# Optimization experiments

Hardware: AMD Instinct MI355X
Metric: run time of the kernel (lower is better)

The kernel has to match this reference:

```python
import jax, jax.numpy as jnp
import numpy as np

DIM, HEADS, B, HT, WD = 96, 8, 4, 160, 160


def conv2d(x, w, b=None, padding=0, groups=1):
    out = jax.lax.conv_general_dilated(
        x, w, (1, 1), [(padding, padding), (padding, padding)],
        dimension_numbers=('NCHW', 'OIHW', 'NCHW'), feature_group_count=groups)
    if b is not None:
        out = out + b[None, :, None, None]
    return out


def setup_inputs() -> dict:
    key = jax.random.key(0)
    ks = jax.random.split(key, 16)
    dim, H = DIM, HEADS
    p = lambda i, shape: jax.random.normal(ks[i], shape, jnp.float32) * 0.05
    return {
        'x': jax.random.normal(ks[0], (B, dim, HT, WD), jnp.float32),
        'spectral': jax.random.normal(ks[1], (B, dim), jnp.float32),
        'temperature': jnp.ones((H, 1, 1), jnp.float32),
        'w_qkv': p(2, (3 * dim, dim, 1, 1)),           # 1x1x1 conv3d == 1x1 conv2d (depth=1)
        'w_dw': p(3, (3 * dim, 1, 3, 3)),              # middle depth slice of 3x3x3 dwconv
        'w_proj': p(4, (dim, dim, 1, 1)),
        'w_fc': p(5, (9, 3 * H)), 'b_fc': jnp.zeros((9,), jnp.float32),
        'w_dep': p(6, (dim, 9, 3, 3)), 'b_dep': jnp.zeros((dim,), jnp.float32),
        'w_se1': p(7, (2 * dim, dim)), 'b_se1': jnp.zeros((2 * dim,), jnp.float32),
        'w_se2': p(8, (dim, 2 * dim)), 'b_se2': jnp.zeros((dim,), jnp.float32),
        'w_saw1': p(9, (dim // 4, 1, 3, 3)), 'b_saw1': jnp.zeros((dim // 4,), jnp.float32),
        'w_saw2': p(10, (HEADS, dim // 4, 1, 1)), 'b_saw2': jnp.zeros((HEADS,), jnp.float32),
        'w_sgp': p(11, (dim, dim)), 'b_sgp': jnp.zeros((dim,), jnp.float32),
    }


def reference(x, spectral, temperature, w_qkv, w_dw, w_proj, w_fc, b_fc,
              w_dep, b_dep, w_se1, b_se1, w_se2, b_se2,
              w_saw1, b_saw1, w_saw2, b_saw2, w_sgp, b_sgp):
    b, c, h, w = x.shape
    H = temperature.shape[0]
    cH = c // H
    # spectral enhance gate: Linear -> GELU -> Linear -> Sigmoid
    sw = jax.nn.sigmoid(
        jax.nn.gelu(spectral @ w_se1.T + b_se1, approximate=False) @ w_se2.T + b_se2)
    x = x * sw[:, :, None, None]
    # qkv: 1x1 conv then 3x3 depthwise (depth-1 3D conv collapses to 2D middle slice)
    qkv = conv2d(conv2d(x, w_qkv), w_dw, padding=1, groups=3 * c)  # (b,3c,h,w)
    # fc branch: reshape (b,3c,h,w) -> (b,hw,3H,cH) -> (b,3H,hw,cH); 1x1 conv over 3H
    f_all = qkv.reshape(b, h * w, 3 * H, cH).transpose(0, 2, 1, 3)
    f_all = jnp.einsum('oc,bcnd->bond', w_fc, f_all) + b_fc[None, :, None, None]  # (b,9,hw,cH)
    f_conv = f_all.transpose(0, 3, 1, 2).reshape(b, 9 * cH, h, w)
    out_conv = conv2d(f_conv, w_dep, b_dep, padding=1, groups=cH)  # (b,c,h,w)
    # channel attention path
    q, k, v = jnp.split(qkv, 3, axis=1)
    resh = lambda t: t.reshape(b, H, cH, h * w)
    q, k, v = resh(q), resh(k), resh(v)
    sg = (spectral @ w_sgp.T + b_sgp).reshape(b, H, cH)
    cm = x.mean(axis=(1, 2, 3), keepdims=True)                      # (b,1,1,1)
    cm_exp = jnp.broadcast_to(cm, (b, 1, h, w))
    saw = jax.nn.sigmoid(conv2d(
        jax.nn.gelu(conv2d(cm_exp, w_saw1, b_saw1, padding=1), approximate=False),
        w_saw2, b_saw2))                                            # (b,H,h,w)
    saw = saw.mean(axis=(2, 3))[..., None]                          # (b,H,1)
    esg = sg * saw                                                  # (b,H,cH)
    sgm = esg[..., :, None] * esg[..., None, :]                     # (b,H,cH,cH)
    qn = q / jnp.maximum(jnp.linalg.norm(q, axis=-1, keepdims=True), 1e-12)
    kn = k / jnp.maximum(jnp.linalg.norm(k, axis=-1, keepdims=True), 1e-12)
    attn = jnp.einsum('bhcn,bhdn->bhcd', qn, kn) * temperature[None]
    attn = jax.nn.softmax(attn * sgm, axis=-1)
    out = jnp.einsum('bhcd,bhdn->bhcn', attn, v).reshape(b, c, h, w)
    out = conv2d(out, w_proj)
    return out + out_conv
```

## Files before the change

### kernel.cpp

```cpp
#include <hip/hip_runtime.h>
#include <math.h>

#define NB 4
#define C 96
#define C3 288
#define NH 8
#define CHD 12
#define HT 160
#define WD 160
#define HW 25600

typedef unsigned short u16;
typedef unsigned int   u32;
typedef __bf16 bf16x8 __attribute__((ext_vector_type(8)));
typedef float  f32x4  __attribute__((ext_vector_type(4)));

__device__ __forceinline__ float gelu_f(float x){
    return 0.5f * x * (1.0f + erff(x * 0.7071067811865475f));
}
__device__ __forceinline__ float sigmoid_f(float x){
    return 1.0f / (1.0f + expf(-x));
}
__device__ __forceinline__ u16 f2bf(float x){
    union { float f; u32 u; } v; v.f = x;
    u32 r = v.u + 0x7FFFu + ((v.u >> 16) & 1u);
    return (u16)(r >> 16);
}
__device__ __forceinline__ float bf2f(u16 s){
    union { u32 u; float f; } v; v.u = ((u32)s) << 16;
    return v.f;
}

__global__ __launch_bounds__(256) void k0_xsum(const float* __restrict__ x,
                                               float* __restrict__ xsum,
                                               u16* __restrict__ xb){
    int bc = blockIdx.x;
    const float4* p4 = (const float4*)(x + (size_t)bc * HW);
    u32* xo = (u32*)(xb + (size_t)bc * HW);
    float s = 0.f;
    for (int i = threadIdx.x; i < HW/4; i += 256){
        float4 v = p4[i];
        s += (v.x + v.y) + (v.z + v.w);
        xo[i*2]   = (u32)f2bf(v.x) | ((u32)f2bf(v.y) << 16);
        xo[i*2+1] = (u32)f2bf(v.z) | ((u32)f2bf(v.w) << 16);
    }
    __shared__ float red[256];
    red[threadIdx.x] = s;
    __syncthreads();
    for (int off = 128; off > 0; off >>= 1){
        if (threadIdx.x < off) red[threadIdx.x] += red[threadIdx.x + off];
        __syncthreads();
    }
    if (threadIdx.x == 0) xsum[bc] = red[0];
}

__global__ void k1_small(const float* __restrict__ spectral, const float* __restrict__ xsum,
                         const float* __restrict__ w_se1, const float* __restrict__ b_se1,
                         const float* __restrict__ w_se2, const float* __restrict__ b_se2,
                         const float* __restrict__ w_saw1, const float* __restrict__ b_saw1,
                         const float* __restrict__ w_saw2, const float* __restrict__ b_saw2,
                         const float* __restrict__ w_sgp, const float* __restrict__ b_sgp,
                         float* __restrict__ swg, float* __restrict__ esgg){
    __shared__ float spec[96];
    __shared__ float h1[192];
    __shared__ float cm_s;
    __shared__ float g1[9][24];
    __shared__ float saw[8];
    __shared__ float redbuf[96];
    int t = threadIdx.x;
    int b = blockIdx.x;
    if (t < 96) spec[t] = spectral[b*96 + t];
    __syncthreads();
    if (t < 192){
        float a = b_se1[t];
        for (int c = 0; c < 96; c++) a += spec[c] * w_se1[t*96 + c];
        h1[t] = gelu_f(a);
    }
    __syncthreads();
    if (t < 96){
        float a = b_se2[t];
        for (int j = 0; j < 192; j++) a += h1[j] * w_se2[t*192 + j];
        float s = sigmoid_f(a);
        swg[b*96 + t] = s;
        redbuf[t] = s * xsum[b*96 + t];
    }
    __syncthreads();
    if (t == 0){
        float cs = 0.f;
        for (int c = 0; c < 96; c++) cs += redbuf[c];
        cm_s = cs / (96.0f * (float)HW);
    }
    __syncthreads();
    float cm = cm_s;
    if (t < 9*24){
        int cat = t / 24, ch = t % 24;
        int ti = cat / 3, tj = cat % 3;
        float S = 0.f;
        for (int ki = 0; ki < 3; ki++){
            if (ti == 0 && ki == 0) continue;
            if (ti == 2 && ki == 2) continue;
            for (int kj = 0; kj < 3; kj++){
                if (tj == 0 && kj == 0) continue;
                if (tj == 2 && kj == 2) continue;
                S += w_saw1[ch*9 + ki*3 + kj];
            }
        }
        g1[cat][ch] = gelu_f(cm * S + b_saw1[ch]);
    }
    __syncthreads();
    if (t < 8){
        float acc = 0.f;
        const float cnt[3] = {1.f, 158.f, 1.f};
        for (int cat = 0; cat < 9; cat++){
            float a = b_saw2[t];
            for (int ch = 0; ch < 24; ch++) a += w_saw2[t*24 + ch] * g1[cat][ch];
            acc += cnt[cat/3] * cnt[cat%3] * sigmoid_f(a);
        }
        saw[t] = acc / (float)HW;
    }
    __syncthreads();
    if (t < 96){
        float a = b_sgp[t];
        for (int j = 0; j < 96; j++) a += spec[j] * w_sgp[t*96 + j];
        esgg[b*96 + t] = a * saw[t/12];
    }
}

__global__ __launch_bounds__(256) void k1w_weff(const float* __restrict__ w_qkv,
                                                const float* __restrict__ swg,
                                                u16* __restrict__ weffb){
    int b = blockIdx.x;
    int i = blockIdx.y * 256 + threadIdx.x;
    float w = w_qkv[i] * swg[b*96 + (i % 96)];
    weffb[(size_t)b*C3*96 + i] = f2bf(w);
}

__global__ __launch_bounds__(384) void k2a_mfma(const u16* __restrict__ xb,
                                                const u16* __restrict__ weffb,
                                                u16* __restrict__ Y,
                                                int bbase, long ystride){
    int b   = bbase + blockIdx.y;
    int px0 = blockIdx.x * 64;
    __shared__ u16 Xl[64*128];
    int t = threadIdx.x;
    const u32* xsrc = (const u32*)(xb + (size_t)b*C*HW + px0);
    for (int i = t; i < 96*32; i += 384){
        int c = i >> 5, pq = i & 31;
        u32 v = xsrc[(size_t)c*(HW/2) + pq];
        int slot = (((c >> 3) ^ (pq & 7)) << 3) + (c & 7);
        Xl[(2*pq)*128 + slot]     = (u16)(v & 0xffffu);
        Xl[(2*pq+1)*128 + slot]   = (u16)(v >> 16);
    }
    int wid = t >> 6, lane = t & 63;
    int lr = lane & 15, lk = lane >> 4;
    union U { uint4 q; bf16x8 v; };
    bf16x8 afr[3][3];
    const u16* wb = weffb + (size_t)b*C3*96;
    #pragma unroll
    for (int og = 0; og < 3; og++){
        int oc = og*96 + wid*16 + lr;
        #pragma unroll
        for (int kk = 0; kk < 3; kk++){
            U u; u.q = *(const uint4*)(wb + (size_t)oc*96 + kk*32 + lk*8);
            afr[og][kk] = u.v;
        }
    }
    __syncthreads();
    u16* Yb = Y + (size_t)blockIdx.y * ystride;
    #pragma unroll
    for (int sub = 0; sub < 4; sub++){
        int px = sub*16 + lr;
        int key = (px >> 1) & 7;
        bf16x8 bfr[3];
        #pragma unroll
        for (int kk = 0; kk < 3; kk++){
            int gs = (kk*4 + lk) ^ key;
            U u; u.q = *(const uint4*)(&Xl[px*128 + gs*8]);
            bfr[kk] = u.v;
        }
        #pragma unroll
        for (int og = 0; og < 3; og++){
            f32x4 acc = (f32x4){0.f,0.f,0.f,0.f};
            #pragma unroll
            for (int kk = 0; kk < 3; kk++)
                acc = __builtin_amdgcn_mfma_f32_16x16x32_bf16(afr[og][kk], bfr[kk], acc, 0, 0, 0);
            #pragma unroll
            for (int r = 0; r < 4; r++){
                int oc = og*96 + wid*16 + lk*4 + r;
                Yb[(size_t)oc*HW + px0 + sub*16 + lr] = f2bf(acc[r]);
            }
        }
    }
}

__global__ __launch_bounds__(256) void k2b_dw(const u16* __restrict__ Y,
                                              const float* __restrict__ w_dw,
                                              u16* __restrict__ qkv,
                                              int bbase, long ystride){
    int b  = bbase + blockIdx.z;
    int ch = blockIdx.y;
    int r0 = blockIdx.x * 8;
    __shared__ float tile[10*162];
    const u16* Yc = Y + (size_t)blockIdx.z*ystride + (size_t)ch*HW;
    int t = threadIdx.x;
    if (t < 10){ tile[t*162] = 0.f; tile[t*162 + 161] = 0.f; }
    for (int i = t; i < 800; i += 256){
        int r = i / 80, c2 = (i % 80) * 2;
        int gr = r0 + r - 1;
        u32 v = 0;
        if (gr >= 0 && gr < HT) v = *(const u32*)(Yc + gr*WD + c2);
        tile[r*162 + 1 + c2] = bf2f((u16)(v & 0xffffu));
        tile[r*162 + 2 + c2] = bf2f((u16)(v >> 16));
    }
    float w[9];
    #pragma unroll
    for (int k = 0; k < 9; k++) w[k] = w_dw[ch*9 + k];
    __syncthreads();
    u16* qc = qkv + ((size_t)b*C3 + ch)*HW + r0*WD;
    for (int i = t; i < 640; i += 256){
        int r = i / 80, c2 = (i % 80) * 2;
        float a0 = 0.f, a1 = 0.f;
        #pragma unroll
        for (int ki = 0; ki < 3; ki++){
            const float* row = &tile[(r+ki)*162 + c2];
            #pragma unroll
            for (int kj = 0; kj < 3; kj++){
                float wv = w[ki*3+kj];
                a0 += wv * row[kj];
                a1 += wv * row[kj+1];
            }
        }
        u32 pk = (u32)f2bf(a0) | ((u32)f2bf(a1) << 16);
        *(u32*)(qc + r*WD + c2) = pk;
    }
}

__global__ __launch_bounds__(256) void k3_mfma(const u16* __restrict__ qkv,
                                               const float* __restrict__ w_fc,
                                               const float* __restrict__ b_fc,
                                               u16* __restrict__ fws){
    int b  = blockIdx.y;
    int n0 = blockIdx.x * 64;
    __shared__ float wfc[216];
    __shared__ float bfc[9];
    __shared__ u16 ot[112*66];
    int t = threadIdx.x;
    if (t < 216) wfc[t] = w_fc[t];
    if (t < 9)   bfc[t] = b_fc[t];
    __syncthreads();
    int wv = t >> 6, lane = t & 63;
    int lr = lane & 15, lk = lane >> 4;
    int nrow = n0 + wv*16 + lr;
    const u16* rowp = qkv + (size_t)b*C3*HW + (size_t)nrow*288;
    union U { uint4 q; bf16x8 v; };
    U bfr[9];
    #pragma unroll
    for (int kk = 0; kk < 9; kk++)
        bfr[kk].q = *(const uint4*)(rowp + kk*32 + lk*8);

    for (int ct = 0; ct < 7; ct++){
        int coA = ct*16 + lr;
        int dA = coA / 9;
        int oA = coA - dA*9;
        f32x4 acc;
        #pragma unroll
        for (int r = 0; r < 4; r++){
            int coD = ct*16 + lk*4 + r;
            acc[r] = (coD < 108) ? bfc[coD % 9] : 0.f;
        }
        #pragma unroll
        for (int kk = 0; kk < 9; kk++){
            int base = kk*32 + lk*8;
            int bm = base % 12;
            int slot = dA - bm; slot += (slot < 0) ? 12 : 0;
            int j = base + slot;
            float wvl = (coA < 108 && slot < 8) ? wfc[oA*24 + j/12] : 0.f;
            u32 pk = ((u32)f2bf(wvl)) << ((slot & 1) * 16);
            int sh = slot >> 1;
            U a;
            a.q.x = (sh == 0) ? pk : 0u;
            a.q.y = (sh == 1) ? pk : 0u;
            a.q.z = (sh == 2) ? pk : 0u;
            a.q.w = (sh == 3) ? pk : 0u;
            acc = __builtin_amdgcn_mfma_f32_16x16x32_bf16(a.v, bfr[kk].v, acc, 0, 0, 0);
        }
        #pragma unroll
        for (int r = 0; r < 4; r++){
            int co = ct*16 + lk*4 + r;
            if (co < 108) ot[co*66 + wv*16 + lr] = f2bf(acc[r]);
        }
    }
    __syncthreads();
    const u32* otp = (const u32*)ot;
    u32* dst = (u32*)(fws + (size_t)b*108*HW + n0);
    for (int i = t; i < 108*32; i += 256){
        int pl = i >> 5, q = i & 31;
        dst[(size_t)pl*(HW/2) + q] = otp[pl*33 + q];
    }
}

__global__ __launch_bounds__(256) void k4_gram(const u16* __restrict__ qkv,
                                               float* __restrict__ gpart){
    int b = blockIdx.z;
    int h = blockIdx.y;
    int t = threadIdx.x;
    __shared__ float qs[12*268];
    __shared__ float ks[12*268];
    const u32* qu = (const u32*)(qkv + ((size_t)b*C3 + h*CHD)*HW + blockIdx.x*1024);
    const u32* ku = (const u32*)(qkv + ((size_t)b*C3 + C + h*CHD)*HW + blockIdx.x*1024);
    float acc = 0.f;
    for (int sc = 0; sc < 4; sc++){
        __syncthreads();
        for (int i = t; i < 12*128; i += 256){
            int rr = i / 128, pu = i % 128;
            u32 qv = qu[rr*(HW/2) + sc*128 + pu];
            u32 kv = ku[rr*(HW/2) + sc*128 + pu];
            qs[rr*268 + 2*pu]     = bf2f((u16)(qv & 0xffffu));
            qs[rr*268 + 2*pu + 1] = bf2f((u16)(qv >> 16));
            ks[rr*268 + 2*pu]     = bf2f((u16)(kv & 0xffffu));
            ks[rr*268 + 2*pu + 1] = bf2f((u16)(kv >> 16));
        }
        __syncthreads();
        if (t < 144){
            int c = t / 12, d = t % 12;
            const float* qq = &qs[c*268];
            const float* kk = &ks[d*268];
            float a = 0.f;
            for (int p = 0; p < 256; p += 4){
                float4 q4 = *(const float4*)(qq + p);
                float4 k4 = *(const float4*)(kk + p);
                a += q4.x*k4.x + q4.y*k4.y + q4.z*k4.z + q4.w*k4.w;
            }
            acc += a;
        } else if (t < 168){
            int c = (t - 144) % 12;
            const float* qq = (t < 156) ? &qs[c*268] : &ks[c*268];
            float a = 0.f;
            for (int p = 0; p < 256; p += 4){
                float4 q4 = *(const float4*)(qq + p);
                a += q4.x*q4.x + q4.y*q4.y + q4.z*q4.z + q4.w*q4.w;
            }
            acc += a;
        }
    }
    if (t < 168)
        gpart[(((size_t)b*NH + h)*25 + blockIdx.x)*168 + t] = acc;
}

__global__ void k5_attn(const float* __restrict__ gpart, const float* __restrict__ esgg,
                        const float* __restrict__ temp, const float* __restrict__ w_proj,
                        u16* __restrict__ Mhib, u16* __restrict__ Mlob){
    int b = blockIdx.x;
    int t = threadIdx.x;
    __shared__ float G[NH][144];
    __shared__ float q2[NH][12], k2[NH][12];
    __shared__ float attn[NH][144];
    for (int i = t; i < NH*168; i += 256){
        int h = i / 168, e = i % 168;
        float a = 0.f;
        for (int ch = 0; ch < 25; ch++)
            a += gpart[(((size_t)b*NH + h)*25 + ch)*168 + e];
        if (e < 144)      G[h][e] = a;
        else if (e < 156) q2[h][e-144] = a;
        else              k2[h][e-156] = a;
    }
    __syncthreads();
    if (t < 96){
        int h = t / 12, c = t % 12;
        float rq  = 1.0f / fmaxf(sqrtf(q2[h][c]), 1e-12f);
        float tm  = temp[h];
        float egc = esgg[b*96 + h*12 + c];
        float lo[12];
        float mx = -1e30f;
        for (int d = 0; d < 12; d++){
            float rk = 1.0f / fmaxf(sqrtf(k2[h][d]), 1e-12f);
            float v = G[h][c*12 + d] * rq * rk * tm * (egc * esgg[b*96 + h*12 + d]);
            lo[d] = v;
            mx = fmaxf(mx, v);
        }
        float s = 0.f;
        for (int d = 0; d < 12; d++){ lo[d] = expf(lo[d] - mx); s += lo[d]; }
        float inv = 1.0f / s;
        for (int d = 0; d < 12; d++) attn[h][c*12 + d] = lo[d] * inv;
    }
    __syncthreads();
    for (int i = t; i < 96*96; i += 256){
        int co = i / 96, ci = i % 96;
        int h = ci / 12, d = ci % 12;
        float a = 0.f;
        #pragma unroll
        for (int c = 0; c < 12; c++)
            a += w_proj[co*96 + h*12 + c] * attn[h][c*12 + d];
        u16 hi = f2bf(a);
        float resid = a - bf2f(hi);
        Mhib[((size_t)b*96 + co)*96 + ci] = hi;
        Mlob[((size_t)b*96 + co)*96 + ci] = f2bf(resid);
    }
}

#define K6_ST 35
#define K6_RT 18
__global__ __launch_bounds__(256) void k6a_mfma(const u16* __restrict__ fws,
                                                const float* __restrict__ w_dep,
                                                const float* __restrict__ b_dep,
                                                float* __restrict__ out){
    int b = blockIdx.z, d = blockIdx.y;
    int ty = blockIdx.x / 5, tx = blockIdx.x % 5;
    int r0 = ty*16, c0 = tx*32;
    __shared__ u16 inl[9*K6_RT*K6_ST];
    __shared__ u16 Wt[16*104];
    __shared__ float bb[8];
    int t = threadIdx.x;
    for (int i = t; i < 9*K6_RT*34; i += 256){
        int ch = i / (K6_RT*34), rem = i % (K6_RT*34), r = rem / 34, cc = rem % 34;
        int gr = r0 + r - 1, gc = c0 + cc - 1;
        u16 v = 0;
        if (gr >= 0 && gr < HT && gc >= 0 && gc < WD)
            v = fws[((size_t)(b*108 + d*9 + ch))*HW + gr*WD + gc];
        inl[(ch*K6_RT + r)*K6_ST + cc] = v;
    }
    for (int i = t; i < 16*96; i += 256){
        int row = i / 96, k = i % 96;
        float wv = (row < 8 && k < 81) ? w_dep[(d*8 + row)*81 + k] : 0.f;
        Wt[row*104 + k] = f2bf(wv);
    }
    if (t < 8) bb[t] = b_dep[d*8 + t];
    __syncthreads();

    int wv = t >> 6, lane = t & 63;
    int lr = lane & 15, lk = lane >> 4;
    union U { uint4 q; bf16x8 v; };
    bf16x8 afr[3];
    #pragma unroll
    for (int kk = 0; kk < 3; kk++){
        U u; u.q = *(const uint4*)(&Wt[lr*104 + kk*32 + lk*8]);
        afr[kk] = u.v;
    }
    int off[3][8];
    #pragma unroll
    for (int kk = 0; kk < 3; kk++)
        #pragma unroll
        for (int j = 0; j < 8; j++){
            int k = kk*32 + lk*8 + j;
            off[kk][j] = (k < 81) ? ((k/9)*K6_RT + (k%9)/3)*K6_ST + (k%3) : 0;
        }
    float binit[4];
    #pragma unroll
    for (int r = 0; r < 4; r++) binit[r] = (lk < 2) ? bb[lk*4 + r] : 0.f;

    for (int gi = 0; gi < 8; gi++){
        int g = wv*8 + gi;
        int ry = g >> 1, half = g & 1;
        int base = ry*K6_ST + half*16 + lr;
        f32x4 acc = (f32x4){binit[0], binit[1], binit[2], binit[3]};
        #pragma unroll
        for (int kk = 0; kk < 3; kk++){
            u16 s0 = inl[base + off[kk][0]];
            u16 s1 = inl[base + off[kk][1]];
            u16 s2 = inl[base + off[kk][2]];
            u16 s3 = inl[base + off[kk][3]];
            u16 s4 = inl[base + off[kk][4]];
            u16 s5 = inl[base + off[kk][5]];
            u16 s6 = inl[base + off[kk][6]];
            u16 s7 = inl[base + off[kk][7]];
            U u;
            u.q.x = (u32)s0 | ((u32)s1 << 16);
            u.q.y = (u32)s2 | ((u32)s3 << 16);
            u.q.z = (u32)s4 | ((u32)s5 << 16);
            u.q.w = (u32)s6 | ((u32)s7 << 16);
            acc = __builtin_amdgcn_mfma_f32_16x16x32_bf16(afr[kk], u.v, acc, 0, 0, 0);
        }
        if (lk < 2){
            #pragma unroll
            for (int r = 0; r < 4; r++){
                int oc = d*8 + lk*4 + r;
                out[((size_t)b*C + oc)*HW + (r0 + ry)*WD + c0 + half*16 + lr] = acc[r];
            }
        }
    }
}

__global__ __launch_bounds__(256) void k6b_mfma(const u16* __restrict__ qkv,
                                                const u16* __restrict__ Mhib,
                                                const u16* __restrict__ Mlob,
                                                float* __restrict__ out){
    int b   = blockIdx.y;
    int px0 = blockIdx.x * 64;
    __shared__ u16 Vl[64*128];
    int t = threadIdx.x;
    const u32* vsrc = (const u32*)(qkv + ((size_t)b*C3 + 2*C)*HW + px0);
    for (int i = t; i < 96*32; i += 256){
        int c = i >> 5, pq = i & 31;
        u32 v = vsrc[(size_t)c*(HW/2) + pq];
        int slot = (((c >> 3) ^ (pq & 7)) << 3) + (c & 7);
        Vl[(2*pq)*128 + slot]   = (u16)(v & 0xffffu);
        Vl[(2*pq+1)*128 + slot] = (u16)(v >> 16);
    }
    __syncthreads();
    int wid = t >> 6, lane = t & 63;
    int lr = lane & 15, lk = lane >> 4;
    union U { uint4 q; bf16x8 v; };
    int px = wid*16 + lr;
    int key = (px >> 1) & 7;
    bf16x8 bfr[3];
    #pragma unroll
    for (int kk = 0; kk < 3; kk++){
        int gs = (kk*4 + lk) ^ key;
        U u; u.q = *(const uint4*)(&Vl[px*128 + gs*8]);
        bfr[kk] = u.v;
    }
    const u16* mh = Mhib + (size_t)b*96*96;
    const u16* ml = Mlob + (size_t)b*96*96;
    for (int og = 0; og < 6; og++){
        int arow = og*16 + lr;
        f32x4 acc = (f32x4){0.f,0.f,0.f,0.f};
        #pragma unroll
        for (int kk = 0; kk < 3; kk++){
            U ah; ah.q = *(const uint4*)(mh + (size_t)arow*96 + kk*32 + lk*8);
            U al; al.q = *(const uint4*)(ml + (size_t)arow*96 + kk*32 + lk*8);
            acc = __builtin_amdgcn_mfma_f32_16x16x32_bf16(ah.v, bfr[kk], acc, 0, 0, 0);
            acc = __builtin_amdgcn_mfma_f32_16x16x32_bf16(al.v, bfr[kk], acc, 0, 0, 0);
        }
        #pragma unroll
        for (int r = 0; r < 4; r++){
            int oc = og*16 + lk*4 + r;
            float* op = out + ((size_t)b*C + oc)*HW + px0 + wid*16 + lr;
            *op += acc[r];
        }
    }
}

extern "C" void kernel_launch(void* const* d_in, const int* in_sizes, int n_in,
                              void* d_out, int out_size, void* d_ws, size_t ws_size,
                              hipStream_t stream){
    (void)in_sizes; (void)n_in; (void)out_size;
    const float* x           = (const float*)d_in[0];
    const float* spectral    = (const float*)d_in[1];
    const float* temperature = (const float*)d_in[2];
    const float* w_qkv       = (const float*)d_in[3];
    const float* w_dw        = (const float*)d_in[4];
    const float* w_proj      = (const float*)d_in[5];
    const float* w_fc        = (const float*)d_in[6];
    const float* b_fc        = (const float*)d_in[7];
    const float* w_dep       = (const float*)d_in[8];
    const float* b_dep       = (const float*)d_in[9];
    const float* w_se1       = (const float*)d_in[10];
    const float* b_se1       = (const float*)d_in[11];
    const float* w_se2       = (const float*)d_in[12];
    const float* b_se2       = (const float*)d_in[13];
    const float* w_saw1      = (const float*)d_in[14];
    const float* b_saw1      = (const float*)d_in[15];
    const float* w_saw2      = (const float*)d_in[16];
    const float* b_saw2      = (const float*)d_in[17];
    const float* w_sgp       = (const float*)d_in[18];
    const float* b_sgp       = (const float*)d_in[19];
    float* out = (float*)d_out;
    char* ws   = (char*)d_ws;

    const size_t QKV_B = 58982400ull;
    const size_t FWS_B = 22118400ull;
    const size_t XB_B  = 19660800ull;
    const size_t SM_B  = 1200000ull;
    const size_t Y_ONE = 14745600ull;
    bool fullY = ws_size >= QKV_B + 4*Y_ONE + FWS_B + XB_B + SM_B;
    size_t ybytes = fullY ? 4*Y_ONE : Y_ONE;

    u16*   qkv = (u16*)ws;
    u16*   Y   = (u16*)(ws + QKV_B);
    u16*   fws = (u16*)(ws + QKV_B + ybytes);
    u16*   xb  = (u16*)(ws + QKV_B + ybytes + FWS_B);
    float* sm  = (float*)(ws + QKV_B + ybytes + FWS_B + XB_B);
    float* xsum  = sm;
    float* swg   = sm + 384;
    float* esgg  = sm + 768;
    float* gpart = sm + 1152;
    u16*   weffb = (u16*)(sm + 135552);
    u16*   Mhib  = (u16*)((char*)weffb + 221184);
    u16*   Mlob  = (u16*)((char*)Mhib + 73728);

    k0_xsum <<<dim3(NB*C), dim3(256), 0, stream>>>(x, xsum, xb);
    k1_small<<<dim3(NB),   dim3(256), 0, stream>>>(spectral, xsum,
                w_se1, b_se1, w_se2, b_se2, w_saw1, b_saw1, w_saw2, b_saw2,
                w_sgp, b_sgp, swg, esgg);
    k1w_weff<<<dim3(NB,108), dim3(256), 0, stream>>>(w_qkv, swg, weffb);
    if (fullY){
        k2a_mfma<<<dim3(400,NB), dim3(384), 0, stream>>>(xb, weffb, Y, 0, (long)C3*HW);
        k2b_dw  <<<dim3(20,C3,NB), dim3(256), 0, stream>>>(Y, w_dw, qkv, 0, (long)C3*HW);
    } else {
        for (int b = 0; b < NB; b++){
            k2a_mfma<<<dim3(400,1), dim3(384), 0, stream>>>(xb, weffb, Y, b, 0);
            k2b_dw  <<<dim3(20,C3,1), dim3(256), 0, stream>>>(Y, w_dw, qkv, b, 0);
        }
    }
    k3_mfma <<<dim3(400,NB),   dim3(256), 0, stream>>>(qkv, w_fc, b_fc, fws);
    k4_gram <<<dim3(25,NH,NB), dim3(256), 0, stream>>>(qkv, gpart);
    k5_attn <<<dim3(NB),       dim3(256), 0, stream>>>(gpart, esgg, temperature, w_proj, Mhib, Mlob);
    k6a_mfma<<<dim3(50,12,NB), dim3(256), 0, stream>>>(fws, w_dep, b_dep, out);
    k6b_mfma<<<dim3(400,NB),   dim3(256), 0, stream>>>(qkv, Mhib, Mlob, out);
}
```

Baseline: 233.3 us.

## Replace MFMA grouped 3x3 conv with direct FP32 register-tiled convolution

The grouped 3x3 conv kernel (k6a) drops its MFMA im2col formulation, which gathered eight scalar bf16 LDS reads per fragment, in favour of a direct FP32 convolution. Each thread now computes a 2x4 pixel block for 4 output channels from a register window loaded as packed u32 reads. Tiles grow to 32x32 and the grid halves, so staging loads are amortized over more outputs and the output is written with float4 stores. The trade-offs are more VALU FMAs in place of matrix-core work, higher register pressure, and weights read from global memory inside the loop.

```diff
diff --git a/kernel.cpp b/kernel.cpp
--- a/kernel.cpp
+++ b/kernel.cpp
@@ -29,6 +29,12 @@
 __device__ __forceinline__ float bf2f(u16 s){
     union { u32 u; float f; } v; v.u = ((u32)s) << 16;
     return v.f;
+}
+__device__ __forceinline__ float lo16(u32 v){
+    union { u32 u; float f; } x; x.u = v << 16; return x.f;
+}
+__device__ __forceinline__ float hi16(u32 v){
+    union { u32 u; float f; } x; x.u = v & 0xffff0000u; return x.f;
 }
 
 __global__ __launch_bounds__(256) void k0_xsum(const float* __restrict__ x,
@@ -398,84 +404,73 @@
     }
 }
 
-#define K6_ST 35
-#define K6_RT 18
-__global__ __launch_bounds__(256) void k6a_mfma(const u16* __restrict__ fws,
-                                                const float* __restrict__ w_dep,
-                                                const float* __restrict__ b_dep,
-                                                float* __restrict__ out){
+__global__ __launch_bounds__(256) void k6a_dir(const u16* __restrict__ fws,
+                                               const float* __restrict__ w_dep,
+                                               const float* __restrict__ b_dep,
+                                               float* __restrict__ out){
     int b = blockIdx.z, d = blockIdx.y;
     int ty = blockIdx.x / 5, tx = blockIdx.x % 5;
-    int r0 = ty*16, c0 = tx*32;
-    __shared__ u16 inl[9*K6_RT*K6_ST];
-    __shared__ u16 Wt[16*104];
-    __shared__ float bb[8];
-    int t = threadIdx.x;
-    for (int i = t; i < 9*K6_RT*34; i += 256){
-        int ch = i / (K6_RT*34), rem = i % (K6_RT*34), r = rem / 34, cc = rem % 34;
-        int gr = r0 + r - 1, gc = c0 + cc - 1;
+    int r0 = ty*32, c0 = tx*32;
+    __shared__ u16 inl[9][34][36];
+    int t = threadIdx.x;
+    for (int i = t; i < 9*34*34; i += 256){
+        int ch = i / 1156, rem = i % 1156, r = rem / 34, c = rem % 34;
+        int gr = r0 + r - 1, gc = c0 + c - 1;
         u16 v = 0;
         if (gr >= 0 && gr < HT && gc >= 0 && gc < WD)
             v = fws[((size_t)(b*108 + d*9 + ch))*HW + gr*WD + gc];
-        inl[(ch*K6_RT + r)*K6_ST + cc] = v;
-    }
-    for (int i = t; i < 16*96; i += 256){
-        int row = i / 96, k = i % 96;
-        float wv = (row < 8 && k < 81) ? w_dep[(d*8 + row)*81 + k] : 0.f;
-        Wt[row*104 + k] = f2bf(wv);
-    }
-    if (t < 8) bb[t] = b_dep[d*8 + t];
-    __syncthreads();
-
-    int wv = t >> 6, lane = t & 63;
-    int lr = lane & 15, lk = lane >> 4;
-    union U { uint4 q; bf16x8 v; };
-    bf16x8 afr[3];
-    #pragma unroll
-    for (int kk = 0; kk < 3; kk++){
-        U u; u.q = *(const uint4*)(&Wt[lr*104 + kk*32 + lk*8]);
-        afr[kk] = u.v;
-    }
-    int off[3][8];
-    #pragma unroll
-    for (int kk = 0; kk < 3; kk++)
-        #pragma unroll
-        for (int j = 0; j < 8; j++){
-            int k = kk*32 + lk*8 + j;
-            off[kk][j] = (k < 81) ? ((k/9)*K6_RT + (k%9)/3)*K6_ST + (k%3) : 0;
-        }
-    float binit[4];
-    #pragma unroll
-    for (int r = 0; r < 4; r++) binit[r] = (lk < 2) ? bb[lk*4 + r] : 0.f;
-
-    for (int gi = 0; gi < 8; gi++){
-        int g = wv*8 + gi;
-        int ry = g >> 1, half = g & 1;
-        int base = ry*K6_ST + half*16 + lr;
-        f32x4 acc = (f32x4){binit[0], binit[1], binit[2], binit[3]};
-        #pragma unroll
-        for (int kk = 0; kk < 3; kk++){
-            u16 s0 = inl[base + off[kk][0]];
-            u16 s1 = inl[base + off[kk][1]];
-            u16 s2 = inl[base + off[kk][2]];
-            u16 s3 = inl[base + off[kk][3]];
-            u16 s4 = inl[base + off[kk][4]];
-            u16 s5 = inl[base + off[kk][5]];
-            u16 s6 = inl[base + off[kk][6]];
-            u16 s7 = inl[base + off[kk][7]];
-            U u;
-            u.q.x = (u32)s0 | ((u32)s1 << 16);
-            u.q.y = (u32)s2 | ((u32)s3 << 16);
-            u.q.z = (u32)s4 | ((u32)s5 << 16);
-            u.q.w = (u32)s6 | ((u32)s7 << 16);
-            acc = __builtin_amdgcn_mfma_f32_16x16x32_bf16(afr[kk], u.v, acc, 0, 0, 0);
-        }
-        if (lk < 2){
+        inl[ch][r][c] = v;
+    }
+    __syncthreads();
+    int wv = __builtin_amdgcn_readfirstlane(t >> 6);
+    int lane = t & 63;
+    int rbase = (wv & 1) * 16;
+    int ocb   = (wv >> 1) * 4;
+    int rp = lane >> 3, cq = lane & 7;
+    const float* wbase = w_dep + (size_t)(d*8 + ocb)*81;
+    float acc[4][8];
+    #pragma unroll
+    for (int oo = 0; oo < 4; oo++){
+        float bv = b_dep[d*8 + ocb + oo];
+        #pragma unroll
+        for (int p = 0; p < 8; p++) acc[oo][p] = bv;
+    }
+    #pragma unroll
+    for (int ch = 0; ch < 9; ch++){
+        float win[4][6];
+        #pragma unroll
+        for (int dr = 0; dr < 4; dr++){
+            int rr = rbase + rp*2 + dr;
+            const u32* p = (const u32*)&inl[ch][rr][cq*4];
+            u32 a = p[0], b2 = p[1], c2 = p[2];
+            win[dr][0] = lo16(a);  win[dr][1] = hi16(a);
+            win[dr][2] = lo16(b2); win[dr][3] = hi16(b2);
+            win[dr][4] = lo16(c2); win[dr][5] = hi16(c2);
+        }
+        #pragma unroll
+        for (int oo = 0; oo < 4; oo++){
+            const float* wp = wbase + oo*81 + ch*9;
             #pragma unroll
-            for (int r = 0; r < 4; r++){
-                int oc = d*8 + lk*4 + r;
-                out[((size_t)b*C + oc)*HW + (r0 + ry)*WD + c0 + half*16 + lr] = acc[r];
-            }
+            for (int ki = 0; ki < 3; ki++)
+                #pragma unroll
+                for (int kj = 0; kj < 3; kj++){
+                    float w = wp[ki*3 + kj];
+                    #pragma unroll
+                    for (int pr = 0; pr < 2; pr++)
+                        #pragma unroll
+                        for (int pc = 0; pc < 4; pc++)
+                            acc[oo][pr*4+pc] += w * win[pr+ki][pc+kj];
+                }
+        }
+    }
+    #pragma unroll
+    for (int oo = 0; oo < 4; oo++){
+        int oc = d*8 + ocb + oo;
+        #pragma unroll
+        for (int pr = 0; pr < 2; pr++){
+            float4 v = make_float4(acc[oo][pr*4+0], acc[oo][pr*4+1],
+                                   acc[oo][pr*4+2], acc[oo][pr*4+3]);
+            *(float4*)(out + ((size_t)b*C + oc)*HW + (r0 + rbase + rp*2 + pr)*WD + c0 + cq*4) = v;
         }
     }
 }
@@ -595,6 +590,6 @@
     k3_mfma <<<dim3(400,NB),   dim3(256), 0, stream>>>(qkv, w_fc, b_fc, fws);
     k4_gram <<<dim3(25,NH,NB), dim3(256), 0, stream>>>(qkv, gpart);
     k5_attn <<<dim3(NB),       dim3(256), 0, stream>>>(gpart, esgg, temperature, w_proj, Mhib, Mlob);
-    k6a_mfma<<<dim3(50,12,NB), dim3(256), 0, stream>>>(fws, w_dep, b_dep, out);
+    k6a_dir <<<dim3(25,12,NB), dim3(256), 0, stream>>>(fws, w_dep, b_dep, out);
     k6b_mfma<<<dim3(400,NB),   dim3(256), 0, stream>>>(qkv, Mhib, Mlob, out);
 }
```

Result: slower. 249.9 us (+7.1%).

## Use MFMA for Gram reduction and tap-major layout in dep conv

Applied to the files above, without the earlier changes.

The per-head q·k Gram and squared-norm reduction moves from scalar fp32 dot products over LDS to bf16 MFMA instructions that read q/k straight from global memory, with a small cross-wave LDS reduction at the end. The grouped 3x3 dep conv stages its input in a channel-innermost LDS layout padded to 24 channels, and the weights are reordered tap-major. Each MFMA B operand then comes from one 16-byte LDS load instead of eight gathered u16 loads. The cost is five MFMAs instead of three because of the zero padding, plus an extra pass to zero LDS. The Gram path also now accumulates norms from bf16 products inside the MFMA.

```diff
diff --git a/kernel.cpp b/kernel.cpp
--- a/kernel.cpp
+++ b/kernel.cpp
@@ -299,52 +299,48 @@
     }
 }
 
-__global__ __launch_bounds__(256) void k4_gram(const u16* __restrict__ qkv,
+__global__ __launch_bounds__(256) void k4_mfma(const u16* __restrict__ qkv,
                                                float* __restrict__ gpart){
-    int b = blockIdx.z;
-    int h = blockIdx.y;
-    int t = threadIdx.x;
-    __shared__ float qs[12*268];
-    __shared__ float ks[12*268];
-    const u32* qu = (const u32*)(qkv + ((size_t)b*C3 + h*CHD)*HW + blockIdx.x*1024);
-    const u32* ku = (const u32*)(qkv + ((size_t)b*C3 + C + h*CHD)*HW + blockIdx.x*1024);
-    float acc = 0.f;
-    for (int sc = 0; sc < 4; sc++){
-        __syncthreads();
-        for (int i = t; i < 12*128; i += 256){
-            int rr = i / 128, pu = i % 128;
-            u32 qv = qu[rr*(HW/2) + sc*128 + pu];
-            u32 kv = ku[rr*(HW/2) + sc*128 + pu];
-            qs[rr*268 + 2*pu]     = bf2f((u16)(qv & 0xffffu));
-            qs[rr*268 + 2*pu + 1] = bf2f((u16)(qv >> 16));
-            ks[rr*268 + 2*pu]     = bf2f((u16)(kv & 0xffffu));
-            ks[rr*268 + 2*pu + 1] = bf2f((u16)(kv >> 16));
-        }
-        __syncthreads();
-        if (t < 144){
-            int c = t / 12, d = t % 12;
-            const float* qq = &qs[c*268];
-            const float* kk = &ks[d*268];
-            float a = 0.f;
-            for (int p = 0; p < 256; p += 4){
-                float4 q4 = *(const float4*)(qq + p);
-                float4 k4 = *(const float4*)(kk + p);
-                a += q4.x*k4.x + q4.y*k4.y + q4.z*k4.z + q4.w*k4.w;
+    int b = blockIdx.z, h = blockIdx.y;
+    int t = threadIdx.x;
+    int wv = t >> 6, lane = t & 63;
+    int lr = lane & 15, lk = lane >> 4;
+    int row = (lr < 12) ? lr : 11;
+    size_t pxb = (size_t)blockIdx.x*1024 + wv*256;
+    const u16* qb = qkv + ((size_t)b*C3 + h*CHD + row)*HW + pxb;
+    const u16* kb = qkv + ((size_t)b*C3 + C + h*CHD + row)*HW + pxb;
+    union U { uint4 q; bf16x8 v; };
+    f32x4 gqk = (f32x4){0.f,0.f,0.f,0.f};
+    f32x4 gqq = (f32x4){0.f,0.f,0.f,0.f};
+    f32x4 gkk = (f32x4){0.f,0.f,0.f,0.f};
+    #pragma unroll
+    for (int s = 0; s < 8; s++){
+        U aq, ak;
+        aq.q = *(const uint4*)(qb + s*32 + lk*8);
+        ak.q = *(const uint4*)(kb + s*32 + lk*8);
+        gqk = __builtin_amdgcn_mfma_f32_16x16x32_bf16(aq.v, ak.v, gqk, 0, 0, 0);
+        gqq = __builtin_amdgcn_mfma_f32_16x16x32_bf16(aq.v, aq.v, gqq, 0, 0, 0);
+        gkk = __builtin_amdgcn_mfma_f32_16x16x32_bf16(ak.v, ak.v, gkk, 0, 0, 0);
+    }
+    __shared__ float red[4][168];
+    for (int i = t; i < 4*168; i += 256) ((float*)red)[i] = 0.f;
+    __syncthreads();
+    #pragma unroll
+    for (int r = 0; r < 4; r++){
+        int c = lk*4 + r;
+        if (lr < 12 && c < 12){
+            red[wv][c*12 + lr] = gqk[r];
+            if (lr == c){
+                red[wv][144 + c] = gqq[r];
+                red[wv][156 + c] = gkk[r];
             }
-            acc += a;
-        } else if (t < 168){
-            int c = (t - 144) % 12;
-            const float* qq = (t < 156) ? &qs[c*268] : &ks[c*268];
-            float a = 0.f;
-            for (int p = 0; p < 256; p += 4){
-                float4 q4 = *(const float4*)(qq + p);
-                a += q4.x*q4.x + q4.y*q4.y + q4.z*q4.z + q4.w*q4.w;
-            }
-            acc += a;
-        }
-    }
-    if (t < 168)
-        gpart[(((size_t)b*NH + h)*25 + blockIdx.x)*168 + t] = acc;
+        }
+    }
+    __syncthreads();
+    if (t < 168){
+        float a = red[0][t] + red[1][t] + red[2][t] + red[3][t];
+        gpart[(((size_t)b*NH + h)*25 + blockIdx.x)*168 + t] = a;
+    }
 }
 
 __global__ void k5_attn(const float* __restrict__ gpart, const float* __restrict__ esgg,
@@ -398,83 +394,67 @@
     }
 }
 
-#define K6_ST 35
-#define K6_RT 18
-__global__ __launch_bounds__(256) void k6a_mfma(const u16* __restrict__ fws,
-                                                const float* __restrict__ w_dep,
-                                                const float* __restrict__ b_dep,
-                                                float* __restrict__ out){
+#define CP6 24
+__global__ __launch_bounds__(256) void k6a_tap(const u16* __restrict__ fws,
+                                               const float* __restrict__ w_dep,
+                                               const float* __restrict__ b_dep,
+                                               float* __restrict__ out){
     int b = blockIdx.z, d = blockIdx.y;
     int ty = blockIdx.x / 5, tx = blockIdx.x % 5;
     int r0 = ty*16, c0 = tx*32;
-    __shared__ u16 inl[9*K6_RT*K6_ST];
-    __shared__ u16 Wt[16*104];
-    __shared__ float bb[8];
-    int t = threadIdx.x;
-    for (int i = t; i < 9*K6_RT*34; i += 256){
-        int ch = i / (K6_RT*34), rem = i % (K6_RT*34), r = rem / 34, cc = rem % 34;
-        int gr = r0 + r - 1, gc = c0 + cc - 1;
+    __shared__ u16 inl[19*34*CP6];
+    __shared__ u16 Wt2[16*160];
+    int t = threadIdx.x;
+    for (int i = t; i < (19*34*CP6)/2; i += 256) ((u32*)inl)[i] = 0u;
+    __syncthreads();
+    for (int i = t; i < 9*18*34; i += 256){
+        int ch = i / 612, rem = i % 612, r = rem / 34, c = rem % 34;
+        int gr = r0 + r - 1, gc = c0 + c - 1;
         u16 v = 0;
         if (gr >= 0 && gr < HT && gc >= 0 && gc < WD)
             v = fws[((size_t)(b*108 + d*9 + ch))*HW + gr*WD + gc];
-        inl[(ch*K6_RT + r)*K6_ST + cc] = v;
-    }
-    for (int i = t; i < 16*96; i += 256){
-        int row = i / 96, k = i % 96;
-        float wv = (row < 8 && k < 81) ? w_dep[(d*8 + row)*81 + k] : 0.f;
-        Wt[row*104 + k] = f2bf(wv);
-    }
-    if (t < 8) bb[t] = b_dep[d*8 + t];
-    __syncthreads();
-
+        inl[(r*34 + c)*CP6 + ch] = v;
+    }
+    for (int i = t; i < 16*160; i += 256){
+        int row = i / 160, k = i % 160;
+        int tap = k >> 4, chp = k & 15;
+        float wv = (row < 8 && tap < 9 && chp < 9)
+                   ? w_dep[(size_t)(d*8 + row)*81 + chp*9 + tap] : 0.f;
+        Wt2[i] = f2bf(wv);
+    }
+    __syncthreads();
     int wv = t >> 6, lane = t & 63;
     int lr = lane & 15, lk = lane >> 4;
     union U { uint4 q; bf16x8 v; };
-    bf16x8 afr[3];
-    #pragma unroll
-    for (int kk = 0; kk < 3; kk++){
-        U u; u.q = *(const uint4*)(&Wt[lr*104 + kk*32 + lk*8]);
+    bf16x8 afr[5];
+    #pragma unroll
+    for (int kk = 0; kk < 5; kk++){
+        U u; u.q = *(const uint4*)(&Wt2[lr*160 + kk*32 + lk*8]);
         afr[kk] = u.v;
     }
-    int off[3][8];
-    #pragma unroll
-    for (int kk = 0; kk < 3; kk++)
-        #pragma unroll
-        for (int j = 0; j < 8; j++){
-            int k = kk*32 + lk*8 + j;
-            off[kk][j] = (k < 81) ? ((k/9)*K6_RT + (k%9)/3)*K6_ST + (k%3) : 0;
-        }
+    int tap0 = lk >> 1;
+    int h8   = (lk & 1) * 8;
     float binit[4];
     #pragma unroll
-    for (int r = 0; r < 4; r++) binit[r] = (lk < 2) ? bb[lk*4 + r] : 0.f;
+    for (int r = 0; r < 4; r++) binit[r] = (lk < 2) ? b_dep[d*8 + lk*4 + r] : 0.f;
 
     for (int gi = 0; gi < 8; gi++){
         int g = wv*8 + gi;
         int ry = g >> 1, half = g & 1;
-        int base = ry*K6_ST + half*16 + lr;
+        int cpx = half*16 + lr;
         f32x4 acc = (f32x4){binit[0], binit[1], binit[2], binit[3]};
         #pragma unroll
-        for (int kk = 0; kk < 3; kk++){
-            u16 s0 = inl[base + off[kk][0]];
-            u16 s1 = inl[base + off[kk][1]];
-            u16 s2 = inl[base + off[kk][2]];
-            u16 s3 = inl[base + off[kk][3]];
-            u16 s4 = inl[base + off[kk][4]];
-            u16 s5 = inl[base + off[kk][5]];
-            u16 s6 = inl[base + off[kk][6]];
-            u16 s7 = inl[base + off[kk][7]];
-            U u;
-            u.q.x = (u32)s0 | ((u32)s1 << 16);
-            u.q.y = (u32)s2 | ((u32)s3 << 16);
-            u.q.z = (u32)s4 | ((u32)s5 << 16);
-            u.q.w = (u32)s6 | ((u32)s7 << 16);
+        for (int kk = 0; kk < 5; kk++){
+            int tap = kk*2 + tap0;
+            int ki = tap / 3, kj = tap - ki*3;
+            U u; u.q = *(const uint4*)(&inl[((ry + ki)*34 + cpx + kj)*CP6 + h8]);
             acc = __builtin_amdgcn_mfma_f32_16x16x32_bf16(afr[kk], u.v, acc, 0, 0, 0);
         }
         if (lk < 2){
             #pragma unroll
             for (int r = 0; r < 4; r++){
                 int oc = d*8 + lk*4 + r;
-                out[((size_t)b*C + oc)*HW + (r0 + ry)*WD + c0 + half*16 + lr] = acc[r];
+                out[((size_t)b*C + oc)*HW + (r0 + ry)*WD + c0 + cpx] = acc[r];
             }
         }
     }
@@ -593,8 +573,8 @@
         }
     }
     k3_mfma <<<dim3(400,NB),   dim3(256), 0, stream>>>(qkv, w_fc, b_fc, fws);
-    k4_gram <<<dim3(25,NH,NB), dim3(256), 0, stream>>>(qkv, gpart);
+    k4_mfma <<<dim3(25,NH,NB), dim3(256), 0, stream>>>(qkv, gpart);
     k5_attn <<<dim3(NB),       dim3(256), 0, stream>>>(gpart, esgg, temperature, w_proj, Mhib, Mlob);
-    k6a_mfma<<<dim3(50,12,NB), dim3(256), 0, stream>>>(fws, w_dep, b_dep, out);
+    k6a_tap <<<dim3(50,12,NB), dim3(256), 0, stream>>>(fws, w_dep, b_dep, out);
     k6b_mfma<<<dim3(400,NB),   dim3(256), 0, stream>>>(qkv, Mhib, Mlob, out);
 }
```

After: 222.7 us. 4.6% less time.
